# Performance work log

Hardware: AMD Instinct MI355X
Metric: run time of the kernel (lower is better)

Reference implementation:

```python
import jax, jax.numpy as jnp
import numpy as np

NORM_EPS = 1e-05

def _quant_input(x):
    # per-token dynamic int8 fake-quant: s = 127 / max(|x|, 1e-5)
    s = 127.0 / jnp.clip(jnp.max(jnp.abs(x), axis=-1, keepdims=True), 1e-05, None)
    return jnp.clip(jnp.round(x * s), -128.0, 127.0) / s

def _rmsnorm(x, w, eps):
    return x * jax.lax.rsqrt(jnp.mean(x * x, axis=-1, keepdims=True) + eps) * w

def setup_inputs() -> dict:
    key = jax.random.key(0)
    k0, k1, k2 = jax.random.split(key, 3)
    dim, hidden = 2048, 5632
    x = jax.random.normal(k0, (4, 2048, dim), dtype=jnp.float32)
    w13 = jax.random.normal(k1, (2 * hidden, dim), dtype=jnp.float32) * 0.02
    w2 = jax.random.normal(k2, (dim, hidden), dtype=jnp.float32) * 0.02
    norm_w = jnp.ones((hidden,), dtype=jnp.float32)
    return {"x": x, "w13": w13, "w2": w2, "norm_w": norm_w}

def reference(x, w13, w2, norm_w):
    # BitLinear w13: quantize input, then linear
    xq = _quant_input(x)
    x13 = jnp.einsum('bsd,fd->bsf', xq, w13)  # [B,S,2H]
    x1, x3 = jnp.split(x13, 2, axis=-1)
    gated = jnp.square(jax.nn.relu(x1)) * x3  # squared-ReLU gating
    inner = _rmsnorm(gated, norm_w, NORM_EPS)
    # BitLinear w2
    iq = _quant_input(inner)
    out = jnp.einsum('bsh,dh->bsd', iq, w2)
    return out
```

## Files before the change

### kernel.cpp

```cpp
#include <hip/hip_runtime.h>

typedef unsigned short u16;
typedef __attribute__((ext_vector_type(8))) short short8;
typedef __attribute__((ext_vector_type(4))) float f32x4;
typedef __attribute__((ext_vector_type(4))) u16 ushort4v;
typedef __attribute__((ext_vector_type(8))) u16 ushort8v;

#define DIM 2048
#define HID 5632
#define F2  11264
#define TTOT 8192

#define GLD(g, l) __builtin_amdgcn_global_load_lds(                       \
    (const __attribute__((address_space(1))) void*)(g),                   \
    (__attribute__((address_space(3))) void*)(l), 16, 0, 0)

__device__ __forceinline__ u16 f2bf(float f) {
  unsigned int u = __builtin_bit_cast(unsigned int, f);
  u += 0x7FFFu + ((u >> 16) & 1u);
  return (u16)(u >> 16);
}

__global__ __launch_bounds__(256) void conv_w13(const float* __restrict__ w,
                                                u16* __restrict__ o) {
  int idx = blockIdx.x * 256 + threadIdx.x;
  int rnew = idx >> 9;
  int dc = (idx & 511) << 2;
  int b = rnew >> 5, ii = rnew & 31;
  int orig = (ii < 16) ? (b * 16 + ii) : (HID + b * 16 + (ii - 16));
  float4 v = *reinterpret_cast<const float4*>(w + (size_t)orig * DIM + dc);
  ushort4v q = {f2bf(v.x), f2bf(v.y), f2bf(v.z), f2bf(v.w)};
  *reinterpret_cast<ushort4v*>(o + (size_t)rnew * DIM + dc) = q;
}

__global__ __launch_bounds__(256) void conv_w2(const float* __restrict__ w,
                                               u16* __restrict__ o) {
  size_t e = ((size_t)blockIdx.x * 256 + threadIdx.x) * 4;
  float4 v = *reinterpret_cast<const float4*>(w + e);
  ushort4v q = {f2bf(v.x), f2bf(v.y), f2bf(v.z), f2bf(v.w)};
  *reinterpret_cast<ushort4v*>(o + e) = q;
}

__global__ __launch_bounds__(256) void quant_x(const float* __restrict__ x,
                                               u16* __restrict__ q,
                                               float* __restrict__ scale) {
  const int t = blockIdx.x;
  const float* xr = x + (size_t)t * DIM;
  const int tid = threadIdx.x;
  float4 a = *reinterpret_cast<const float4*>(xr + tid * 8);
  float4 b = *reinterpret_cast<const float4*>(xr + tid * 8 + 4);
  float v[8] = {a.x, a.y, a.z, a.w, b.x, b.y, b.z, b.w};
  float m = 0.f;
#pragma unroll
  for (int i = 0; i < 8; ++i) m = fmaxf(m, fabsf(v[i]));
#pragma unroll
  for (int off = 32; off; off >>= 1) m = fmaxf(m, __shfl_xor(m, off));
  __shared__ float red[4];
  if ((tid & 63) == 0) red[tid >> 6] = m;
  __syncthreads();
  m = fmaxf(fmaxf(red[0], red[1]), fmaxf(red[2], red[3]));
  m = fmaxf(m, 1e-5f);
  float s = 127.0f / m;
  if (tid == 0) scale[t] = m / 127.0f;
  ushort8v o;
#pragma unroll
  for (int i = 0; i < 8; ++i) {
    float r = fminf(fmaxf(rintf(v[i] * s), -128.f), 127.f);
    o[i] = f2bf(r);
  }
  *reinterpret_cast<ushort8v*>(q + (size_t)t * DIM + tid * 8) = o;
}

__global__ __launch_bounds__(256) void gate_nq(const float* __restrict__ G,
                                               const float* __restrict__ nw,
                                               u16* __restrict__ q2,
                                               float* __restrict__ s2) {
  const int t = blockIdx.x;
  const float* gr = G + (size_t)t * HID;
  const int tid = threadIdx.x;
  float4 vv[6];
  float ss = 0.f, mx = 0.f;
#pragma unroll
  for (int k = 0; k < 6; ++k) {
    int i = tid + k * 256;
    if (i < 1408) {
      float4 v = *reinterpret_cast<const float4*>(gr + i * 4);
      float4 w4 = *reinterpret_cast<const float4*>(nw + i * 4);
      vv[k] = v;
      ss += v.x * v.x + v.y * v.y + v.z * v.z + v.w * v.w;
      mx = fmaxf(mx, fmaxf(fmaxf(fabsf(v.x * w4.x), fabsf(v.y * w4.y)),
                           fmaxf(fabsf(v.z * w4.z), fabsf(v.w * w4.w))));
    }
  }
#pragma unroll
  for (int off = 32; off; off >>= 1) {
    ss += __shfl_xor(ss, off);
    mx = fmaxf(mx, __shfl_xor(mx, off));
  }
  __shared__ float rs[4], rm[4];
  if ((tid & 63) == 0) { rs[tid >> 6] = ss; rm[tid >> 6] = mx; }
  __syncthreads();
  ss = rs[0] + rs[1] + rs[2] + rs[3];
  mx = fmaxf(fmaxf(rm[0], rm[1]), fmaxf(rm[2], rm[3]));
  float rinv = 1.0f / sqrtf(ss * (1.0f / 5632.0f) + 1e-5f);
  float mi = fmaxf(mx * rinv, 1e-5f);
  float s = 127.0f / mi;
  if (tid == 0) s2[t] = mi / 127.0f;
  float fs = rinv * s;
#pragma unroll
  for (int k = 0; k < 6; ++k) {
    int i = tid + k * 256;
    if (i < 1408) {
      float4 v = vv[k];
      float4 w4 = *reinterpret_cast<const float4*>(nw + i * 4);
      ushort4v o;
      o.x = f2bf(fminf(fmaxf(rintf(v.x * w4.x * fs), -128.f), 127.f));
      o.y = f2bf(fminf(fmaxf(rintf(v.y * w4.y * fs), -128.f), 127.f));
      o.z = f2bf(fminf(fmaxf(rintf(v.z * w4.z * fs), -128.f), 127.f));
      o.w = f2bf(fminf(fmaxf(rintf(v.w * w4.w * fs), -128.f), 127.f));
      *reinterpret_cast<ushort4v*>(q2 + (size_t)t * HID + i * 4) = o;
    }
  }
}

template <int GATE>
__global__ __launch_bounds__(512, 2) void gemm8(
    const u16* __restrict__ A, const u16* __restrict__ B,
    const float* __restrict__ rowscale, float* __restrict__ C,
    int N, int K, int Ntiles) {
  __shared__ __attribute__((aligned(16))) u16 lds[2][2][2][256 * 32];
  const int NT = K >> 6;
  const int nwg = gridDim.x;
  const int orig = blockIdx.x;
  const int qq = nwg >> 3, rr = nwg & 7, xcd = orig & 7, sidx = orig >> 3;
  const int wg = (xcd < rr ? xcd * (qq + 1) : rr * (qq + 1) + (xcd - rr) * qq) + sidx;
  const int mt = wg / Ntiles, nt = wg % Ntiles;

  const int tid = threadIdx.x;
  const int wid = tid >> 6, lane = tid & 63;
  const int wm = wid >> 2, wn = wid & 3;
  const int c16 = lane & 15, q4 = lane >> 4;
  const int rA_base = wm * 128 + c16;
  const int rB_base = wn * 64 + c16;
  const int caf = (q4 ^ ((lane >> 1) & 3)) << 3;

  const int sr = tid >> 2;
  const int scol = ((tid & 3) ^ ((tid >> 3) & 3)) << 3;
  const u16* Ar = A + ((size_t)mt * 256 + sr) * K + scol;
  const u16* Br = B + ((size_t)nt * 256 + sr) * K + scol;
  const size_t rstep = (size_t)128 * K;

  f32x4 acc[8][4];
#pragma unroll
  for (int m = 0; m < 8; ++m)
#pragma unroll
    for (int n = 0; n < 4; ++n) acc[m][n] = f32x4{0.f, 0.f, 0.f, 0.f};

  auto stage = [&](int mat, int kk, int t) {
    if (t < NT) {
      const u16* g = (mat ? Br : Ar) + t * 64 + kk * 32;
      u16* l = &lds[t & 1][mat][kk][wid << 9];
      GLD(g, l);
      GLD(g + rstep, l + 4096);
    }
  };
  auto ldA = [&](int db, int kk, int mh, short8* af) {
#pragma unroll
    for (int m = 0; m < 4; ++m)
      af[m] = *reinterpret_cast<const short8*>(
          &lds[db][0][kk][(rA_base + (mh * 4 + m) * 16) * 32 + caf]);
  };
  auto ldB = [&](int db, int kk, short8* bfr) {
#pragma unroll
    for (int n = 0; n < 4; ++n)
      bfr[n] = *reinterpret_cast<const short8*>(
          &lds[db][1][kk][(rB_base + n * 16) * 32 + caf]);
  };

#define MFMA16(AF, BF, OFS)                                                   \
  __builtin_amdgcn_s_setprio(1);                                              \
  _Pragma("unroll") for (int m = 0; m < 4; ++m)                               \
      _Pragma("unroll") for (int n = 0; n < 4; ++n)                           \
          acc[(OFS) + m][n] = __builtin_amdgcn_mfma_f32_16x16x32_bf16(        \
              AF[m], BF[n], acc[(OFS) + m][n], 0, 0, 0);                      \
  __builtin_amdgcn_s_setprio(0);                                              \
  __builtin_amdgcn_sched_barrier(0);

  stage(1, 0, 0); stage(0, 0, 0); stage(1, 1, 0); stage(0, 1, 0);
  stage(1, 0, 1); stage(0, 0, 1); stage(1, 1, 1);
  asm volatile("s_waitcnt vmcnt(6)" ::: "memory");
  asm volatile("s_barrier" ::: "memory");

  short8 af_a[4], af_b[4], bf_a[4], bf_b[4];
  ldB(0, 0, bf_a);
  ldA(0, 0, 0, af_a);

  for (int u = 0; u < NT; ++u) {
    const int db = u & 1;
    stage(0, 1, u + 1);
    asm volatile("s_barrier" ::: "memory");
    ldA(db, 0, 1, af_b);
    __builtin_amdgcn_sched_barrier(0);
    MFMA16(af_a, bf_a, 0)
    asm volatile("s_barrier" ::: "memory");
    stage(1, 0, u + 2);
    asm volatile("s_barrier" ::: "memory");
    ldB(db, 1, bf_b);
    ldA(db, 1, 0, af_a);
    __builtin_amdgcn_sched_barrier(0);
    MFMA16(af_b, bf_a, 4)
    asm volatile("s_barrier" ::: "memory");
    stage(0, 0, u + 2);
    asm volatile("s_barrier" ::: "memory");
    ldA(db, 1, 1, af_b);
    __builtin_amdgcn_sched_barrier(0);
    MFMA16(af_a, bf_b, 0)
    asm volatile("s_barrier" ::: "memory");
    stage(1, 1, u + 2);
    if (u + 2 < NT) asm volatile("s_waitcnt vmcnt(6)" ::: "memory");
    else            asm volatile("s_waitcnt vmcnt(0)" ::: "memory");
    asm volatile("s_barrier" ::: "memory");
    if (u + 1 < NT) {
      ldB(db ^ 1, 0, bf_a);
      ldA(db ^ 1, 0, 0, af_a);
    }
    __builtin_amdgcn_sched_barrier(0);
    MFMA16(af_b, bf_b, 4)
    asm volatile("s_barrier" ::: "memory");
  }

  const int mbase0 = mt * 256 + wm * 128;
  if constexpr (GATE == 0) {
#pragma unroll
    for (int m = 0; m < 8; ++m) {
#pragma unroll
      for (int j = 0; j < 4; ++j) {
        const int row = mbase0 + m * 16 + q4 * 4 + j;
        const float sc = rowscale[row];
        float* crow = C + (size_t)row * N + nt * 256 + wn * 64 + c16;
#pragma unroll
        for (int n = 0; n < 4; ++n) crow[n * 16] = acc[m][n][j] * sc;
      }
    }
  } else {
    const int H = N >> 1;
    const int gbase = (nt * 256 + wn * 64) >> 1;
#pragma unroll
    for (int m = 0; m < 8; ++m) {
#pragma unroll
      for (int j = 0; j < 4; ++j) {
        const int row = mbase0 + m * 16 + q4 * 4 + j;
        const float sc = rowscale[row];
        const float s3 = sc * sc * sc;
        float* grow = C + (size_t)row * H + gbase + c16;
#pragma unroll
        for (int p = 0; p < 2; ++p) {
          float a1 = acc[m][2 * p][j];
          float a3 = acc[m][2 * p + 1][j];
          float rl = fmaxf(a1, 0.f);
          grow[p * 16] = rl * rl * a3 * s3;
        }
      }
    }
  }
}

extern "C" void kernel_launch(void* const* d_in, const int* in_sizes, int n_in,
                              void* d_out, int out_size, void* d_ws, size_t ws_size,
                              hipStream_t stream) {
  const float* x = (const float*)d_in[0];
  const float* w13 = (const float*)d_in[1];
  const float* w2 = (const float*)d_in[2];
  const float* nw = (const float*)d_in[3];
  float* out = (float*)d_out;

  char* p = (char*)d_ws;
  u16* w13p = (u16*)p; p += (size_t)F2 * DIM * 2;
  u16* w2b = (u16*)p;  p += (size_t)DIM * HID * 2;
  u16* q2f = (u16*)p;  p += (size_t)TTOT * HID * 2;
  float* s2f = (float*)p; p += (size_t)TTOT * 4;
  const size_t fixed = (size_t)F2 * DIM * 2 + (size_t)DIM * HID * 2 +
                       (size_t)TTOT * HID * 2 + (size_t)TTOT * 4;
  const size_t perTok = (size_t)DIM * 2 + (size_t)HID * 4 + 8;
  int Tc = TTOT;
  while (Tc > 256 && fixed + (size_t)Tc * perTok > ws_size) Tc >>= 1;
  u16* q1 = (u16*)p;        p += (size_t)Tc * DIM * 2;
  float* gated = (float*)p; p += (size_t)Tc * HID * 4;
  float* s1 = (float*)p;

  conv_w13<<<F2 * DIM / 4 / 256, 256, 0, stream>>>(w13, w13p);
  conv_w2<<<DIM * HID / 4 / 256, 256, 0, stream>>>(w2, w2b);

  for (int t0 = 0; t0 < TTOT; t0 += Tc) {
    quant_x<<<Tc, 256, 0, stream>>>(x + (size_t)t0 * DIM, q1, s1);
    gemm8<1><<<(Tc / 256) * (F2 / 256), 512, 0, stream>>>(q1, w13p, s1, gated,
                                                          F2, DIM, F2 / 256);
    gate_nq<<<Tc, 256, 0, stream>>>(gated, nw, q2f + (size_t)t0 * HID, s2f + t0);
  }
  gemm8<0><<<(TTOT / 256) * (DIM / 256), 512, 0, stream>>>(q2f, w2b, s2f, out,
                                                           DIM, HID, DIM / 256);
}
```

Measured before the change: 643.1 us.

## Switch GEMM to 32x32x16 MFMA with reworked fragment loads and k-loop

Replaces the 16x16x32 bf16 MFMA tiles with 32x32x16 MFMA, changing accumulator layout, LDS fragment addressing, and epilogue row/column mapping. The w13 interleave is widened to 32-row groups so gate/up pairs line up with the new 32-column output blocks. The main loop is unrolled by two k-tiles with explicit buffer indices and now loads fragments just before each MFMA group rather than prefetching across stages. The larger MFMA shape cuts LDS fragment traffic per flop, at the cost of less load/compute overlap inside each wave, and it assumes NT is even.

```diff
diff --git a/kernel.cpp b/kernel.cpp
--- a/kernel.cpp
+++ b/kernel.cpp
@@ -2,7 +2,7 @@
 
 typedef unsigned short u16;
 typedef __attribute__((ext_vector_type(8))) short short8;
-typedef __attribute__((ext_vector_type(4))) float f32x4;
+typedef __attribute__((ext_vector_type(16))) float f32x16;
 typedef __attribute__((ext_vector_type(4))) u16 ushort4v;
 typedef __attribute__((ext_vector_type(8))) u16 ushort8v;
 
@@ -26,8 +26,8 @@
   int idx = blockIdx.x * 256 + threadIdx.x;
   int rnew = idx >> 9;
   int dc = (idx & 511) << 2;
-  int b = rnew >> 5, ii = rnew & 31;
-  int orig = (ii < 16) ? (b * 16 + ii) : (HID + b * 16 + (ii - 16));
+  int b = rnew >> 6, ii = rnew & 63;
+  int orig = (ii < 32) ? (b * 32 + ii) : (HID + b * 32 + (ii - 32));
   float4 v = *reinterpret_cast<const float4*>(w + (size_t)orig * DIM + dc);
   ushort4v q = {f2bf(v.x), f2bf(v.y), f2bf(v.z), f2bf(v.w)};
   *reinterpret_cast<ushort4v*>(o + (size_t)rnew * DIM + dc) = q;
@@ -139,10 +139,12 @@
   const int tid = threadIdx.x;
   const int wid = tid >> 6, lane = tid & 63;
   const int wm = wid >> 2, wn = wid & 3;
-  const int c16 = lane & 15, q4 = lane >> 4;
-  const int rA_base = wm * 128 + c16;
-  const int rB_base = wn * 64 + c16;
-  const int caf = (q4 ^ ((lane >> 1) & 3)) << 3;
+  const int r31 = lane & 31, q2 = lane >> 5;
+  const int p = (lane >> 1) & 3;
+  const int offq0 = ((0 * 2 + q2) ^ p) << 3;
+  const int offq1 = ((1 * 2 + q2) ^ p) << 3;
+  const int aBase = (wm * 128 + r31) * 32;
+  const int bBase = (wn * 64 + r31) * 32;
 
   const int sr = tid >> 2;
   const int scol = ((tid & 3) ^ ((tid >> 3) & 3)) << 3;
@@ -150,116 +152,121 @@
   const u16* Br = B + ((size_t)nt * 256 + sr) * K + scol;
   const size_t rstep = (size_t)128 * K;
 
-  f32x4 acc[8][4];
-#pragma unroll
-  for (int m = 0; m < 8; ++m)
-#pragma unroll
-    for (int n = 0; n < 4; ++n) acc[m][n] = f32x4{0.f, 0.f, 0.f, 0.f};
-
-  auto stage = [&](int mat, int kk, int t) {
+  f32x16 acc[4][2];
+#pragma unroll
+  for (int mb = 0; mb < 4; ++mb)
+#pragma unroll
+    for (int nb = 0; nb < 2; ++nb)
+#pragma unroll
+      for (int e = 0; e < 16; ++e) acc[mb][nb][e] = 0.f;
+
+  auto stage = [&](int mat, int kk, int t, int buf) {
     if (t < NT) {
       const u16* g = (mat ? Br : Ar) + t * 64 + kk * 32;
-      u16* l = &lds[t & 1][mat][kk][wid << 9];
+      u16* l = &lds[buf][mat][kk][wid << 9];
       GLD(g, l);
       GLD(g + rstep, l + 4096);
     }
   };
-  auto ldA = [&](int db, int kk, int mh, short8* af) {
-#pragma unroll
-    for (int m = 0; m < 4; ++m)
-      af[m] = *reinterpret_cast<const short8*>(
-          &lds[db][0][kk][(rA_base + (mh * 4 + m) * 16) * 32 + caf]);
-  };
-  auto ldB = [&](int db, int kk, short8* bfr) {
-#pragma unroll
-    for (int n = 0; n < 4; ++n)
-      bfr[n] = *reinterpret_cast<const short8*>(
-          &lds[db][1][kk][(rB_base + n * 16) * 32 + caf]);
-  };
-
-#define MFMA16(AF, BF, OFS)                                                   \
+
+#define LDA32(DB, KK, MH, AF)                                                 \
+  {                                                                           \
+    const u16* pa = &lds[DB][0][KK][0] + aBase + (MH) * 2048;                 \
+    AF[0] = *reinterpret_cast<const short8*>(pa + offq0);                     \
+    AF[1] = *reinterpret_cast<const short8*>(pa + offq1);                     \
+    AF[2] = *reinterpret_cast<const short8*>(pa + 1024 + offq0);              \
+    AF[3] = *reinterpret_cast<const short8*>(pa + 1024 + offq1);              \
+  }
+#define LDB32(DB, KK, BF)                                                     \
+  {                                                                           \
+    const u16* pb = &lds[DB][1][KK][0] + bBase;                               \
+    BF[0] = *reinterpret_cast<const short8*>(pb + offq0);                     \
+    BF[1] = *reinterpret_cast<const short8*>(pb + offq1);                     \
+    BF[2] = *reinterpret_cast<const short8*>(pb + 1024 + offq0);              \
+    BF[3] = *reinterpret_cast<const short8*>(pb + 1024 + offq1);              \
+  }
+#define MFMA8(AF, BF, MBOFS)                                                  \
   __builtin_amdgcn_s_setprio(1);                                              \
-  _Pragma("unroll") for (int m = 0; m < 4; ++m)                               \
-      _Pragma("unroll") for (int n = 0; n < 4; ++n)                           \
-          acc[(OFS) + m][n] = __builtin_amdgcn_mfma_f32_16x16x32_bf16(        \
-              AF[m], BF[n], acc[(OFS) + m][n], 0, 0, 0);                      \
+  _Pragma("unroll") for (int ks = 0; ks < 2; ++ks)                            \
+      _Pragma("unroll") for (int mb2 = 0; mb2 < 2; ++mb2)                     \
+          _Pragma("unroll") for (int nb = 0; nb < 2; ++nb)                    \
+              acc[(MBOFS) + mb2][nb] = __builtin_amdgcn_mfma_f32_32x32x16_bf16( \
+                  AF[mb2 * 2 + ks], BF[nb * 2 + ks], acc[(MBOFS) + mb2][nb],  \
+                  0, 0, 0);                                                   \
   __builtin_amdgcn_s_setprio(0);                                              \
   __builtin_amdgcn_sched_barrier(0);
-
-  stage(1, 0, 0); stage(0, 0, 0); stage(1, 1, 0); stage(0, 1, 0);
-  stage(1, 0, 1); stage(0, 0, 1); stage(1, 1, 1);
+#define BARR asm volatile("s_barrier" ::: "memory")
+
+#define KTILE(DB, U)                                                          \
+  {                                                                           \
+    short8 af[4], bfr[4];                                                     \
+                                                      \
+    LDB32(DB, 0, bfr);                                                        \
+    LDA32(DB, 0, 0, af);                                                      \
+    stage(0, 1, (U) + 1, DB ^ 1);                                             \
+    BARR;                                                                     \
+    MFMA8(af, bfr, 0)                                                         \
+    BARR;                                                                     \
+                                                      \
+    LDA32(DB, 0, 1, af);                                                      \
+    stage(1, 0, (U) + 2, DB);                                                 \
+    BARR;                                                                     \
+    MFMA8(af, bfr, 2)                                                         \
+    BARR;                                                                     \
+                                                      \
+    LDB32(DB, 1, bfr);                                                        \
+    LDA32(DB, 1, 0, af);                                                      \
+    stage(0, 0, (U) + 2, DB);                                                 \
+    BARR;                                                                     \
+    MFMA8(af, bfr, 0)                                                         \
+    BARR;                                                                     \
+                                                      \
+    LDA32(DB, 1, 1, af);                                                      \
+    stage(1, 1, (U) + 2, DB);                                                 \
+    if ((U) + 2 < NT) asm volatile("s_waitcnt vmcnt(6)" ::: "memory");        \
+    else              asm volatile("s_waitcnt vmcnt(0)" ::: "memory");        \
+    BARR;                                                                     \
+    MFMA8(af, bfr, 2)                                                         \
+    BARR;                                                                     \
+  }
+
+  stage(1, 0, 0, 0); stage(0, 0, 0, 0); stage(1, 1, 0, 0); stage(0, 1, 0, 0);
+  stage(1, 0, 1, 1); stage(0, 0, 1, 1); stage(1, 1, 1, 1);
   asm volatile("s_waitcnt vmcnt(6)" ::: "memory");
-  asm volatile("s_barrier" ::: "memory");
-
-  short8 af_a[4], af_b[4], bf_a[4], bf_b[4];
-  ldB(0, 0, bf_a);
-  ldA(0, 0, 0, af_a);
-
-  for (int u = 0; u < NT; ++u) {
-    const int db = u & 1;
-    stage(0, 1, u + 1);
-    asm volatile("s_barrier" ::: "memory");
-    ldA(db, 0, 1, af_b);
-    __builtin_amdgcn_sched_barrier(0);
-    MFMA16(af_a, bf_a, 0)
-    asm volatile("s_barrier" ::: "memory");
-    stage(1, 0, u + 2);
-    asm volatile("s_barrier" ::: "memory");
-    ldB(db, 1, bf_b);
-    ldA(db, 1, 0, af_a);
-    __builtin_amdgcn_sched_barrier(0);
-    MFMA16(af_b, bf_a, 4)
-    asm volatile("s_barrier" ::: "memory");
-    stage(0, 0, u + 2);
-    asm volatile("s_barrier" ::: "memory");
-    ldA(db, 1, 1, af_b);
-    __builtin_amdgcn_sched_barrier(0);
-    MFMA16(af_a, bf_b, 0)
-    asm volatile("s_barrier" ::: "memory");
-    stage(1, 1, u + 2);
-    if (u + 2 < NT) asm volatile("s_waitcnt vmcnt(6)" ::: "memory");
-    else            asm volatile("s_waitcnt vmcnt(0)" ::: "memory");
-    asm volatile("s_barrier" ::: "memory");
-    if (u + 1 < NT) {
-      ldB(db ^ 1, 0, bf_a);
-      ldA(db ^ 1, 0, 0, af_a);
-    }
-    __builtin_amdgcn_sched_barrier(0);
-    MFMA16(af_b, bf_b, 4)
-    asm volatile("s_barrier" ::: "memory");
+  BARR;
+
+  for (int u = 0; u < NT; u += 2) {
+    KTILE(0, u)
+    KTILE(1, u + 1)
   }
 
   const int mbase0 = mt * 256 + wm * 128;
   if constexpr (GATE == 0) {
 #pragma unroll
-    for (int m = 0; m < 8; ++m) {
-#pragma unroll
-      for (int j = 0; j < 4; ++j) {
-        const int row = mbase0 + m * 16 + q4 * 4 + j;
+    for (int mb = 0; mb < 4; ++mb) {
+#pragma unroll
+      for (int reg = 0; reg < 16; ++reg) {
+        const int row = mbase0 + mb * 32 + (reg & 3) + 8 * (reg >> 2) + 4 * q2;
         const float sc = rowscale[row];
-        float* crow = C + (size_t)row * N + nt * 256 + wn * 64 + c16;
-#pragma unroll
-        for (int n = 0; n < 4; ++n) crow[n * 16] = acc[m][n][j] * sc;
+        float* crow = C + (size_t)row * N + nt * 256 + wn * 64 + r31;
+        crow[0]  = acc[mb][0][reg] * sc;
+        crow[32] = acc[mb][1][reg] * sc;
       }
     }
   } else {
     const int H = N >> 1;
-    const int gbase = (nt * 256 + wn * 64) >> 1;
-#pragma unroll
-    for (int m = 0; m < 8; ++m) {
-#pragma unroll
-      for (int j = 0; j < 4; ++j) {
-        const int row = mbase0 + m * 16 + q4 * 4 + j;
+    const int gcol = nt * 128 + wn * 32 + r31;
+#pragma unroll
+    for (int mb = 0; mb < 4; ++mb) {
+#pragma unroll
+      for (int reg = 0; reg < 16; ++reg) {
+        const int row = mbase0 + mb * 32 + (reg & 3) + 8 * (reg >> 2) + 4 * q2;
         const float sc = rowscale[row];
         const float s3 = sc * sc * sc;
-        float* grow = C + (size_t)row * H + gbase + c16;
-#pragma unroll
-        for (int p = 0; p < 2; ++p) {
-          float a1 = acc[m][2 * p][j];
-          float a3 = acc[m][2 * p + 1][j];
-          float rl = fmaxf(a1, 0.f);
-          grow[p * 16] = rl * rl * a3 * s3;
-        }
+        float a1 = acc[mb][0][reg];
+        float a3 = acc[mb][1][reg];
+        float rl = fmaxf(a1, 0.f);
+        C[(size_t)row * H + gcol] = rl * rl * a3 * s3;
       }
     }
   }
```

After: 674.6 us. 1.05x slower.

## Drop register double-buffering of LDS fragments and halve barriers in GEMM loop

Applied to the files above, without the earlier changes.

Replaces the ping-pong register fragments (af_a/af_b, bf_a/bf_b), which prefetched the next LDS fragments while MFMAs ran, with a single fragment set that is loaded right before each MFMA block. The number of s_barriers per iteration drops from eight to four, and the sched_barrier fences between loads and MFMAs are removed. The aim is lower synchronisation overhead and fewer registers. The cost is that LDS read latency is no longer hidden behind the previous MFMA group, which may stall the matrix units. The added BARR before each ldA/ldB write into af/bfr is also fewer than before, which could raise LDS race concerns with stage() overwriting buffers.

```diff
diff --git a/kernel.cpp b/kernel.cpp
--- a/kernel.cpp
+++ b/kernel.cpp
@@ -185,48 +185,36 @@
               AF[m], BF[n], acc[(OFS) + m][n], 0, 0, 0);                      \
   __builtin_amdgcn_s_setprio(0);                                              \
   __builtin_amdgcn_sched_barrier(0);
+#define BARR asm volatile("s_barrier" ::: "memory")
 
   stage(1, 0, 0); stage(0, 0, 0); stage(1, 1, 0); stage(0, 1, 0);
   stage(1, 0, 1); stage(0, 0, 1); stage(1, 1, 1);
   asm volatile("s_waitcnt vmcnt(6)" ::: "memory");
-  asm volatile("s_barrier" ::: "memory");
-
-  short8 af_a[4], af_b[4], bf_a[4], bf_b[4];
-  ldB(0, 0, bf_a);
-  ldA(0, 0, 0, af_a);
+  BARR;
 
   for (int u = 0; u < NT; ++u) {
     const int db = u & 1;
+    short8 af[4], bfr[4];
+    ldB(db, 0, bfr);
+    ldA(db, 0, 0, af);
     stage(0, 1, u + 1);
-    asm volatile("s_barrier" ::: "memory");
-    ldA(db, 0, 1, af_b);
-    __builtin_amdgcn_sched_barrier(0);
-    MFMA16(af_a, bf_a, 0)
-    asm volatile("s_barrier" ::: "memory");
+    MFMA16(af, bfr, 0)
+    BARR;
+    ldA(db, 0, 1, af);
     stage(1, 0, u + 2);
-    asm volatile("s_barrier" ::: "memory");
-    ldB(db, 1, bf_b);
-    ldA(db, 1, 0, af_a);
-    __builtin_amdgcn_sched_barrier(0);
-    MFMA16(af_b, bf_a, 4)
-    asm volatile("s_barrier" ::: "memory");
+    MFMA16(af, bfr, 4)
+    BARR;
+    ldB(db, 1, bfr);
+    ldA(db, 1, 0, af);
     stage(0, 0, u + 2);
-    asm volatile("s_barrier" ::: "memory");
-    ldA(db, 1, 1, af_b);
-    __builtin_amdgcn_sched_barrier(0);
-    MFMA16(af_a, bf_b, 0)
-    asm volatile("s_barrier" ::: "memory");
+    MFMA16(af, bfr, 0)
+    BARR;
+    ldA(db, 1, 1, af);
     stage(1, 1, u + 2);
+    MFMA16(af, bfr, 4)
     if (u + 2 < NT) asm volatile("s_waitcnt vmcnt(6)" ::: "memory");
     else            asm volatile("s_waitcnt vmcnt(0)" ::: "memory");
-    asm volatile("s_barrier" ::: "memory");
-    if (u + 1 < NT) {
-      ldB(db ^ 1, 0, bf_a);
-      ldA(db ^ 1, 0, 0, af_a);
-    }
-    __builtin_amdgcn_sched_barrier(0);
-    MFMA16(af_b, bf_b, 4)
-    asm volatile("s_barrier" ::: "memory");
+    BARR;
   }
 
   const int mbase0 = mt * 256 + wm * 128;
```

Measured after the change: 608.8 us. 5.3% less time.
